# Kernel tuning notes

Hardware: AMD Instinct MI355X
Metric: run time of the kernel (lower is better)

## Reference

```python
import jax, jax.numpy as jnp
import numpy as np

B, N, DIN, DOUT = 4, 4096, 512, 128
NEG_INF = -1.0e9  # matches torch's -1000000000.0 fill


def setup_inputs() -> dict:
    key = jax.random.key(0)
    k1, k2, k3, k4 = jax.random.split(key, 4)
    x = jax.random.normal(k1, (B, N, DIN), dtype=jnp.float32)
    adj = (jax.random.uniform(k2, (N, N)) < 0.004).astype(jnp.float32)
    # xavier_uniform with gain=sqrt(2) for weights
    lim_w = float(np.sqrt(2.0) * np.sqrt(6.0 / (DIN + DOUT)))
    weights = jax.random.uniform(k3, (DIN, DOUT), jnp.float32, -lim_w, lim_w)
    # xavier_uniform (gain=1) for a: shape [2*DOUT, 1]
    lim_a = float(np.sqrt(6.0 / (2 * DOUT + 1)))
    a = jax.random.uniform(k4, (2 * DOUT, 1), jnp.float32, -lim_a, lim_a)
    return {"x": x, "adj": adj, "weights": weights, "a": a}


def reference(x, adj, weights, a):
    d = weights.shape[1]
    a_src = a[:d]   # [D, 1]
    a_dst = a[d:]   # [D, 1]

    def per_graph(xs):  # xs: [N, DIN]
        wh = xs @ weights                      # [N, D]
        e = wh @ a_src + (wh @ a_dst).T        # [N,1] + [1,N] -> [N,N]
        e = jnp.where(e > 0, e, 0.01 * e)      # LeakyReLU(0.01)
        att = jax.nn.softmax(jnp.where(adj > 0, e, NEG_INF), axis=1)
        out = att @ wh                          # [N, D]
        return adj @ out                        # sparse-adj mm (dense here)

    return jax.nn.relu(jax.vmap(per_graph)(x))  # act = ReLU
```

## Files before the change

### kernel.cpp

```cpp
#include <hip/hip_runtime.h>
#include <cstdint>
#include <cstddef>

#define BATCH 4
#define NNODE 4096
#define DIN   512
#define DOUT  128
#define CAP   64

#define WH_BLOCKS 1024

typedef __attribute__((ext_vector_type(8))) short bf16x8;
typedef __attribute__((ext_vector_type(4))) float f32x4;
typedef __attribute__((ext_vector_type(4))) unsigned short us4;

static __device__ __forceinline__ unsigned short f2bf_rne(float f) {
    union { float f; uint32_t u; } v; v.f = f;
    uint32_t u = v.u;
    uint32_t r = u + 0x7FFFu + ((u >> 16) & 1u);
    return (unsigned short)(r >> 16);
}
static __device__ __forceinline__ float bf2f(unsigned short h) {
    union { float f; uint32_t u; } v; v.u = ((uint32_t)h) << 16;
    return v.f;
}

__global__ __launch_bounds__(256) void k_wt(const float* __restrict__ W,
                                            unsigned short* __restrict__ Wt) {
    int t = threadIdx.x;
    int i0 = blockIdx.x * 1024;
#pragma unroll
    for (int r = 0; r < 4; ++r) {
        int i = i0 + r * 256 + t;
        int n = i >> 9;
        int k = i & (DIN - 1);
        Wt[i] = f2bf_rne(W[(size_t)k * DOUT + n]);
    }
}

__global__ __launch_bounds__(256) void k_main(const float* __restrict__ x,
                                              const float* __restrict__ adj,
                                              const unsigned short* __restrict__ Wt,
                                              const float* __restrict__ a,
                                              unsigned short* __restrict__ wh,
                                              float* __restrict__ sv,
                                              float* __restrict__ dvv,
                                              float* __restrict__ colpart,
                                              int* __restrict__ nbr_cnt,
                                              int* __restrict__ nbr_idx) {
    __shared__ float lacc[4][8][64][4];
    __shared__ int pref[256];
    int t = threadIdx.x;
    int w = t >> 6;
    int l = t & 63;
    int bid = blockIdx.x;

    if (bid % 5 == 0) {
        int rowbase = (bid / 5) * 16;
        int row = rowbase + (l & 15);
        int kq = w * 128 + ((l >> 4) << 3);
        f32x4 acc[8] = {};
        const float* xrow = x + (size_t)row * DIN + kq;
        const unsigned short* wb = Wt + kq;
#pragma unroll
        for (int ks = 0; ks < 4; ++ks) {
            float4 a0 = *(const float4*)(xrow + ks * 32);
            float4 a1 = *(const float4*)(xrow + ks * 32 + 4);
            float af[8] = {a0.x,a0.y,a0.z,a0.w,a1.x,a1.y,a1.z,a1.w};
            bf16x8 ah, al;
#pragma unroll
            for (int i = 0; i < 8; ++i) {
                unsigned short hh = f2bf_rne(af[i]);
                ah[i] = (short)hh;
                al[i] = (short)f2bf_rne(af[i] - bf2f(hh));
            }
#pragma unroll
            for (int ni = 0; ni < 8; ++ni) {
                bf16x8 b = *(const bf16x8*)(wb + (size_t)(ni*16 + (l & 15)) * DIN + ks * 32);
                acc[ni] = __builtin_amdgcn_mfma_f32_16x16x32_bf16(ah, b, acc[ni], 0, 0, 0);
                acc[ni] = __builtin_amdgcn_mfma_f32_16x16x32_bf16(al, b, acc[ni], 0, 0, 0);
            }
        }
#pragma unroll
        for (int ni = 0; ni < 8; ++ni)
            *(f32x4*)&lacc[w][ni][l][0] = acc[ni];
        __syncthreads();

        int row4 = rowbase + ((l >> 4) << 2);
#pragma unroll
        for (int q = 0; q < 2; ++q) {
            int ni = w * 2 + q;
            f32x4 sum = *(const f32x4*)&lacc[0][ni][l][0];
            sum += *(const f32x4*)&lacc[1][ni][l][0];
            sum += *(const f32x4*)&lacc[2][ni][l][0];
            sum += *(const f32x4*)&lacc[3][ni][l][0];
            int col = ni*16 + (l & 15);
#pragma unroll
            for (int r = 0; r < 4; ++r)
                wh[(size_t)(row4 + r) * DOUT + col] = f2bf_rne(sum[r]);
            float rs = sum[0] + sum[1] + sum[2] + sum[3];
            rs += __shfl_xor(rs, 16, 64);
            rs += __shfl_xor(rs, 32, 64);
            if (l < 16) colpart[(size_t)(bid / 5) * DOUT + ni*16 + l] = rs;
        }
        if (w == 0) {
            float sp[4] = {0,0,0,0}, dp[4] = {0,0,0,0};
#pragma unroll
            for (int ni = 0; ni < 8; ++ni) {
                f32x4 sum = *(const f32x4*)&lacc[0][ni][l][0];
                sum += *(const f32x4*)&lacc[1][ni][l][0];
                sum += *(const f32x4*)&lacc[2][ni][l][0];
                sum += *(const f32x4*)&lacc[3][ni][l][0];
                int col = ni*16 + (l & 15);
                float as = a[col], ad = a[DOUT + col];
#pragma unroll
                for (int r = 0; r < 4; ++r) {
                    sp[r] += sum[r] * as;
                    dp[r] += sum[r] * ad;
                }
            }
#pragma unroll
            for (int off = 1; off <= 8; off <<= 1) {
#pragma unroll
                for (int r = 0; r < 4; ++r) {
                    sp[r] += __shfl_xor(sp[r], off, 64);
                    dp[r] += __shfl_xor(dp[r], off, 64);
                }
            }
            if ((l & 15) == 0) {
#pragma unroll
                for (int r = 0; r < 4; ++r) {
                    sv[row4 + r] = sp[r];
                    dvv[row4 + r] = dp[r];
                }
            }
        }
    } else {
        int row = bid - bid / 5 - 1;
        const float4* p = (const float4*)(adj + (size_t)row * NNODE) + t * 4;
        unsigned mask = 0;
#pragma unroll
        for (int q = 0; q < 4; ++q) {
            float4 v = p[q];
            mask |= (v.x > 0.f ? 1u : 0u) << (q*4+0);
            mask |= (v.y > 0.f ? 1u : 0u) << (q*4+1);
            mask |= (v.z > 0.f ? 1u : 0u) << (q*4+2);
            mask |= (v.w > 0.f ? 1u : 0u) << (q*4+3);
        }
        int cnt = __popc(mask);
        pref[t] = cnt;
        __syncthreads();
        for (int off = 1; off < 256; off <<= 1) {
            int v = pref[t];
            int add = (t >= off) ? pref[t - off] : 0;
            __syncthreads();
            pref[t] = v + add;
            __syncthreads();
        }
        int total = pref[255];
        int base = pref[t] - cnt;
        int cbase = t * 16;
        while (mask) {
            int b = __ffs(mask) - 1;
            mask &= mask - 1;
            if (base < CAP) nbr_idx[row * CAP + base] = cbase + b;
            ++base;
        }
        if (t == 0) nbr_cnt[row] = total > CAP ? CAP : total;
    }
}

__global__ __launch_bounds__(256) void k_att(const unsigned short* __restrict__ wh,
                                             const float* __restrict__ s,
                                             const float* __restrict__ dv,
                                             const int* __restrict__ nbr_cnt,
                                             const int* __restrict__ nbr_idx,
                                             const float* __restrict__ colpart,
                                             unsigned short* __restrict__ out) {
    int bswz = (int)(((blockIdx.x & 7) << 9) | (blockIdx.x >> 3));
    int gid = bswz * 4 + (threadIdx.x >> 6);
    int l = threadIdx.x & 63;
    int b = gid >> 12;
    int i = gid & (NNODE - 1);
    int bb = b << 12;
    int c = nbr_cnt[i];
    int j = (l < c) ? nbr_idx[i * CAP + l] : 0;
    float p = 0.f;
    if (l < c) {
        float ev = s[gid] + dv[bb + j];
        ev = ev > 0.f ? ev : 0.01f * ev;
        p = __expf(ev);
    }
    float den = p;
#pragma unroll
    for (int off = 32; off >= 1; off >>= 1) den += __shfl_xor(den, off, 64);
    int half = l >> 5;
    int lc = l & 31;
    float4 acc = {0.f, 0.f, 0.f, 0.f};
    if (c > 0) {
        for (int jj = 0; jj < c; jj += 8) {
            int s0 = jj + half,     s1 = jj + 2 + half;
            int s2 = jj + 4 + half, s3 = jj + 6 + half;
            int jv0 = __shfl(j, s0, 64); float pv0 = __shfl(p, s0, 64);
            int jv1 = __shfl(j, s1, 64); float pv1 = __shfl(p, s1, 64);
            int jv2 = __shfl(j, s2, 64); float pv2 = __shfl(p, s2, 64);
            int jv3 = __shfl(j, s3, 64); float pv3 = __shfl(p, s3, 64);
            us4 v0 = *((const us4*)(wh + (size_t)(bb + jv0) * DOUT) + lc);
            us4 v1 = *((const us4*)(wh + (size_t)(bb + jv1) * DOUT) + lc);
            us4 v2 = *((const us4*)(wh + (size_t)(bb + jv2) * DOUT) + lc);
            us4 v3 = *((const us4*)(wh + (size_t)(bb + jv3) * DOUT) + lc);
            acc.x += pv0*bf2f(v0[0]) + pv1*bf2f(v1[0]) + pv2*bf2f(v2[0]) + pv3*bf2f(v3[0]);
            acc.y += pv0*bf2f(v0[1]) + pv1*bf2f(v1[1]) + pv2*bf2f(v2[1]) + pv3*bf2f(v3[1]);
            acc.z += pv0*bf2f(v0[2]) + pv1*bf2f(v1[2]) + pv2*bf2f(v2[2]) + pv3*bf2f(v3[2]);
            acc.w += pv0*bf2f(v0[3]) + pv1*bf2f(v1[3]) + pv2*bf2f(v2[3]) + pv3*bf2f(v3[3]);
        }
        acc.x += __shfl_xor(acc.x, 32, 64);
        acc.y += __shfl_xor(acc.y, 32, 64);
        acc.z += __shfl_xor(acc.z, 32, 64);
        acc.w += __shfl_xor(acc.w, 32, 64);
        float inv = 1.f / den;
        acc.x *= inv; acc.y *= inv; acc.z *= inv; acc.w *= inv;
    } else {
        const float inv_n = 1.f / (float)NNODE;
        for (int gg = 0; gg < 256; ++gg) {
            const float* cp = colpart + (size_t)((b << 8) + gg) * DOUT + lc*4;
            acc.x += cp[0]; acc.y += cp[1]; acc.z += cp[2]; acc.w += cp[3];
        }
        acc.x *= inv_n; acc.y *= inv_n; acc.z *= inv_n; acc.w *= inv_n;
    }
    if (half == 0) {
        us4 o;
        o[0] = f2bf_rne(acc.x); o[1] = f2bf_rne(acc.y);
        o[2] = f2bf_rne(acc.z); o[3] = f2bf_rne(acc.w);
        *((us4*)(out + (size_t)gid * DOUT) + lc) = o;
    }
}

__global__ __launch_bounds__(256) void k_agg(const unsigned short* __restrict__ out,
                                             const int* __restrict__ nbr_cnt,
                                             const int* __restrict__ nbr_idx,
                                             float* __restrict__ y) {
    int bswz = (int)(((blockIdx.x & 7) << 9) | (blockIdx.x >> 3));
    int gid = bswz * 4 + (threadIdx.x >> 6);
    int l = threadIdx.x & 63;
    int b = gid >> 12;
    int i = gid & (NNODE - 1);
    int bb = b << 12;
    int c = nbr_cnt[i];
    int j = (l < c) ? nbr_idx[i * CAP + l] : 0;
    float wt = (l < c) ? 1.f : 0.f;
    int half = l >> 5;
    int lc = l & 31;
    float4 acc = {0.f, 0.f, 0.f, 0.f};
    for (int jj = 0; jj < c; jj += 8) {
        int s0 = jj + half,     s1 = jj + 2 + half;
        int s2 = jj + 4 + half, s3 = jj + 6 + half;
        int jv0 = __shfl(j, s0, 64); float pv0 = __shfl(wt, s0, 64);
        int jv1 = __shfl(j, s1, 64); float pv1 = __shfl(wt, s1, 64);
        int jv2 = __shfl(j, s2, 64); float pv2 = __shfl(wt, s2, 64);
        int jv3 = __shfl(j, s3, 64); float pv3 = __shfl(wt, s3, 64);
        us4 v0 = *((const us4*)(out + (size_t)(bb + jv0) * DOUT) + lc);
        us4 v1 = *((const us4*)(out + (size_t)(bb + jv1) * DOUT) + lc);
        us4 v2 = *((const us4*)(out + (size_t)(bb + jv2) * DOUT) + lc);
        us4 v3 = *((const us4*)(out + (size_t)(bb + jv3) * DOUT) + lc);
        acc.x += pv0*bf2f(v0[0]) + pv1*bf2f(v1[0]) + pv2*bf2f(v2[0]) + pv3*bf2f(v3[0]);
        acc.y += pv0*bf2f(v0[1]) + pv1*bf2f(v1[1]) + pv2*bf2f(v2[1]) + pv3*bf2f(v3[1]);
        acc.z += pv0*bf2f(v0[2]) + pv1*bf2f(v1[2]) + pv2*bf2f(v2[2]) + pv3*bf2f(v3[2]);
        acc.w += pv0*bf2f(v0[3]) + pv1*bf2f(v1[3]) + pv2*bf2f(v2[3]) + pv3*bf2f(v3[3]);
    }
    acc.x += __shfl_xor(acc.x, 32, 64);
    acc.y += __shfl_xor(acc.y, 32, 64);
    acc.z += __shfl_xor(acc.z, 32, 64);
    acc.w += __shfl_xor(acc.w, 32, 64);
    acc.x = fmaxf(acc.x, 0.f); acc.y = fmaxf(acc.y, 0.f);
    acc.z = fmaxf(acc.z, 0.f); acc.w = fmaxf(acc.w, 0.f);
    if (half == 0)
        *((float4*)(y + (size_t)gid * DOUT) + lc) = acc;
}

extern "C" void kernel_launch(void* const* d_in, const int* in_sizes, int n_in,
                              void* d_out, int out_size, void* d_ws, size_t ws_size,
                              hipStream_t stream) {
    const float* x   = (const float*)d_in[0];
    const float* adj = (const float*)d_in[1];
    const float* W   = (const float*)d_in[2];
    const float* a   = (const float*)d_in[3];
    float* y = (float*)d_out;

    char* ws = (char*)d_ws;
    size_t o = 0;
    int*            nbr_cnt = (int*)(ws + o);            o += (size_t)NNODE * 4;
    int*            nbr_idx = (int*)(ws + o);            o += (size_t)NNODE * CAP * 4;
    unsigned short* Wt      = (unsigned short*)(ws + o); o += (size_t)DOUT * DIN * 2;
    unsigned short* wh      = (unsigned short*)(ws + o); o += (size_t)BATCH * NNODE * DOUT * 2;
    float*          sv      = (float*)(ws + o);          o += (size_t)BATCH * NNODE * 4;
    float*          dvv     = (float*)(ws + o);          o += (size_t)BATCH * NNODE * 4;
    float*          colpart = (float*)(ws + o);          o += (size_t)WH_BLOCKS * DOUT * 4;
    unsigned short* outbuf  = (unsigned short*)(ws + o); o += (size_t)BATCH * NNODE * DOUT * 2;

    k_wt  <<<64, 256, 0, stream>>>(W, Wt);
    k_main<<<WH_BLOCKS + NNODE, 256, 0, stream>>>(x, adj, Wt, a, wh, sv, dvv,
                                                  colpart, nbr_cnt, nbr_idx);
    k_att <<<(BATCH*NNODE)/4, 256, 0, stream>>>(wh, sv, dvv, nbr_cnt, nbr_idx, colpart, outbuf);
    k_agg <<<(BATCH*NNODE)/4, 256, 0, stream>>>(outbuf, nbr_cnt, nbr_idx, y);
}
```

Baseline: 169.8 us.

## Shrink fused projection/adjacency blocks to 128 threads with wave-level scan

The fused k_main kernel now runs 128-thread blocks. The projection path splits K across two waves instead of four, which halves the LDS reduction buffer, and each wave computes its share of the attention dot products before a small LDS combine. The adjacency path handles two rows per block with one wave per row. Each lane scans 64 columns into a 64-bit mask and computes prefix offsets with wave shuffles instead of a 256-thread LDS scan with many barriers. This aims to cut barrier and LDS overhead and to rebalance the work; in exchange each thread issues more loads and holds more registers.

Result: slower. 182.1 us (+7.2%).

```diff
diff --git a/kernel.cpp b/kernel.cpp
--- a/kernel.cpp
+++ b/kernel.cpp
@@ -8,8 +8,6 @@
 #define DOUT  128
 #define CAP   64
 
-#define WH_BLOCKS 1024
-
 typedef __attribute__((ext_vector_type(8))) short bf16x8;
 typedef __attribute__((ext_vector_type(4))) float f32x4;
 typedef __attribute__((ext_vector_type(4))) unsigned short us4;
@@ -38,7 +36,7 @@
     }
 }
 
-__global__ __launch_bounds__(256) void k_main(const float* __restrict__ x,
+__global__ __launch_bounds__(128) void k_main(const float* __restrict__ x,
                                               const float* __restrict__ adj,
                                               const unsigned short* __restrict__ Wt,
                                               const float* __restrict__ a,
@@ -48,22 +46,23 @@
                                               float* __restrict__ colpart,
                                               int* __restrict__ nbr_cnt,
                                               int* __restrict__ nbr_idx) {
-    __shared__ float lacc[4][8][64][4];
-    __shared__ int pref[256];
+    __shared__ float lacc[2][4][64][4];
+    __shared__ float sdbuf[2][4][4][2];
     int t = threadIdx.x;
     int w = t >> 6;
     int l = t & 63;
     int bid = blockIdx.x;
 
-    if (bid % 5 == 0) {
-        int rowbase = (bid / 5) * 16;
+    if (bid % 3 == 0) {
+        int g = bid / 3;
+        int rowbase = g * 16;
         int row = rowbase + (l & 15);
-        int kq = w * 128 + ((l >> 4) << 3);
+        int kq = w * 256 + ((l >> 4) << 3);
         f32x4 acc[8] = {};
         const float* xrow = x + (size_t)row * DIN + kq;
         const unsigned short* wb = Wt + kq;
 #pragma unroll
-        for (int ks = 0; ks < 4; ++ks) {
+        for (int ks = 0; ks < 8; ++ks) {
             float4 a0 = *(const float4*)(xrow + ks * 32);
             float4 a1 = *(const float4*)(xrow + ks * 32 + 4);
             float af[8] = {a0.x,a0.y,a0.z,a0.w,a1.x,a1.y,a1.z,a1.w};
@@ -81,92 +80,84 @@
                 acc[ni] = __builtin_amdgcn_mfma_f32_16x16x32_bf16(al, b, acc[ni], 0, 0, 0);
             }
         }
-#pragma unroll
-        for (int ni = 0; ni < 8; ++ni)
-            *(f32x4*)&lacc[w][ni][l][0] = acc[ni];
+        int oh = 1 - w;
+#pragma unroll
+        for (int q = 0; q < 4; ++q)
+            *(f32x4*)&lacc[w][q][l][0] = acc[oh*4 + q];
         __syncthreads();
 
+        float sp[4] = {0,0,0,0}, dp[4] = {0,0,0,0};
         int row4 = rowbase + ((l >> 4) << 2);
 #pragma unroll
-        for (int q = 0; q < 2; ++q) {
-            int ni = w * 2 + q;
-            f32x4 sum = *(const f32x4*)&lacc[0][ni][l][0];
-            sum += *(const f32x4*)&lacc[1][ni][l][0];
-            sum += *(const f32x4*)&lacc[2][ni][l][0];
-            sum += *(const f32x4*)&lacc[3][ni][l][0];
+        for (int q = 0; q < 4; ++q) {
+            int ni = w*4 + q;
+            f32x4 sum = acc[ni];
+            sum += *(const f32x4*)&lacc[oh][q][l][0];
             int col = ni*16 + (l & 15);
-#pragma unroll
-            for (int r = 0; r < 4; ++r)
+            float as = a[col], ad = a[DOUT + col];
+#pragma unroll
+            for (int r = 0; r < 4; ++r) {
+                sp[r] += sum[r] * as;
+                dp[r] += sum[r] * ad;
                 wh[(size_t)(row4 + r) * DOUT + col] = f2bf_rne(sum[r]);
+            }
             float rs = sum[0] + sum[1] + sum[2] + sum[3];
             rs += __shfl_xor(rs, 16, 64);
             rs += __shfl_xor(rs, 32, 64);
-            if (l < 16) colpart[(size_t)(bid / 5) * DOUT + ni*16 + l] = rs;
-        }
-        if (w == 0) {
-            float sp[4] = {0,0,0,0}, dp[4] = {0,0,0,0};
-#pragma unroll
-            for (int ni = 0; ni < 8; ++ni) {
-                f32x4 sum = *(const f32x4*)&lacc[0][ni][l][0];
-                sum += *(const f32x4*)&lacc[1][ni][l][0];
-                sum += *(const f32x4*)&lacc[2][ni][l][0];
-                sum += *(const f32x4*)&lacc[3][ni][l][0];
-                int col = ni*16 + (l & 15);
-                float as = a[col], ad = a[DOUT + col];
-#pragma unroll
-                for (int r = 0; r < 4; ++r) {
-                    sp[r] += sum[r] * as;
-                    dp[r] += sum[r] * ad;
-                }
-            }
-#pragma unroll
-            for (int off = 1; off <= 8; off <<= 1) {
-#pragma unroll
-                for (int r = 0; r < 4; ++r) {
-                    sp[r] += __shfl_xor(sp[r], off, 64);
-                    dp[r] += __shfl_xor(dp[r], off, 64);
-                }
-            }
-            if ((l & 15) == 0) {
-#pragma unroll
-                for (int r = 0; r < 4; ++r) {
-                    sv[row4 + r] = sp[r];
-                    dvv[row4 + r] = dp[r];
-                }
-            }
+            if (l < 16) colpart[(size_t)g * DOUT + ni*16 + l] = rs;
+        }
+#pragma unroll
+        for (int off = 1; off <= 8; off <<= 1) {
+#pragma unroll
+            for (int r = 0; r < 4; ++r) {
+                sp[r] += __shfl_xor(sp[r], off, 64);
+                dp[r] += __shfl_xor(dp[r], off, 64);
+            }
+        }
+        if ((l & 15) == 0) {
+#pragma unroll
+            for (int r = 0; r < 4; ++r) {
+                sdbuf[w][l >> 4][r][0] = sp[r];
+                sdbuf[w][l >> 4][r][1] = dp[r];
+            }
+        }
+        __syncthreads();
+        if (w == 0 && l < 16) {
+            float s_ = sdbuf[0][l >> 2][l & 3][0] + sdbuf[1][l >> 2][l & 3][0];
+            float d_ = sdbuf[0][l >> 2][l & 3][1] + sdbuf[1][l >> 2][l & 3][1];
+            sv[rowbase + l] = s_;
+            dvv[rowbase + l] = d_;
         }
     } else {
-        int row = bid - bid / 5 - 1;
-        const float4* p = (const float4*)(adj + (size_t)row * NNODE) + t * 4;
-        unsigned mask = 0;
-#pragma unroll
-        for (int q = 0; q < 4; ++q) {
+        int idx = bid - bid / 3 - 1;
+        int row = idx * 2 + w;
+        const float4* p = (const float4*)(adj + (size_t)row * NNODE) + l * 16;
+        unsigned long long mask = 0ull;
+#pragma unroll
+        for (int q = 0; q < 16; ++q) {
             float4 v = p[q];
-            mask |= (v.x > 0.f ? 1u : 0u) << (q*4+0);
-            mask |= (v.y > 0.f ? 1u : 0u) << (q*4+1);
-            mask |= (v.z > 0.f ? 1u : 0u) << (q*4+2);
-            mask |= (v.w > 0.f ? 1u : 0u) << (q*4+3);
-        }
-        int cnt = __popc(mask);
-        pref[t] = cnt;
-        __syncthreads();
-        for (int off = 1; off < 256; off <<= 1) {
-            int v = pref[t];
-            int add = (t >= off) ? pref[t - off] : 0;
-            __syncthreads();
-            pref[t] = v + add;
-            __syncthreads();
-        }
-        int total = pref[255];
-        int base = pref[t] - cnt;
-        int cbase = t * 16;
+            mask |= (v.x > 0.f ? 1ull : 0ull) << (q*4+0);
+            mask |= (v.y > 0.f ? 1ull : 0ull) << (q*4+1);
+            mask |= (v.z > 0.f ? 1ull : 0ull) << (q*4+2);
+            mask |= (v.w > 0.f ? 1ull : 0ull) << (q*4+3);
+        }
+        int cnt = __popcll(mask);
+        int incl = cnt;
+#pragma unroll
+        for (int off = 1; off < 64; off <<= 1) {
+            int o = __shfl_up(incl, off, 64);
+            if (l >= off) incl += o;
+        }
+        int base = incl - cnt;
+        int total = __shfl(incl, 63, 64);
+        int cbase = l * 64;
         while (mask) {
-            int b = __ffs(mask) - 1;
+            int b = __ffsll(mask) - 1;
             mask &= mask - 1;
             if (base < CAP) nbr_idx[row * CAP + base] = cbase + b;
             ++base;
         }
-        if (t == 0) nbr_cnt[row] = total > CAP ? CAP : total;
+        if (l == 0) nbr_cnt[row] = total > CAP ? CAP : total;
     }
 }
 
@@ -295,12 +286,12 @@
     unsigned short* wh      = (unsigned short*)(ws + o); o += (size_t)BATCH * NNODE * DOUT * 2;
     float*          sv      = (float*)(ws + o);          o += (size_t)BATCH * NNODE * 4;
     float*          dvv     = (float*)(ws + o);          o += (size_t)BATCH * NNODE * 4;
-    float*          colpart = (float*)(ws + o);          o += (size_t)WH_BLOCKS * DOUT * 4;
+    float*          colpart = (float*)(ws + o);          o += (size_t)1024 * DOUT * 4;
     unsigned short* outbuf  = (unsigned short*)(ws + o); o += (size_t)BATCH * NNODE * DOUT * 2;
 
     k_wt  <<<64, 256, 0, stream>>>(W, Wt);
-    k_main<<<WH_BLOCKS + NNODE, 256, 0, stream>>>(x, adj, Wt, a, wh, sv, dvv,
-                                                  colpart, nbr_cnt, nbr_idx);
+    k_main<<<3072, 128, 0, stream>>>(x, adj, Wt, a, wh, sv, dvv,
+                                     colpart, nbr_cnt, nbr_idx);
     k_att <<<(BATCH*NNODE)/4, 256, 0, stream>>>(wh, sv, dvv, nbr_cnt, nbr_idx, colpart, outbuf);
     k_agg <<<(BATCH*NNODE)/4, 256, 0, stream>>>(outbuf, nbr_cnt, nbr_idx, y);
 }
```
